# Performance work log

Measured on AMD Instinct MI355X. Metric: run time of the kernel, lower is better.

Reference implementation:

```python
import jax, jax.numpy as jnp
import numpy as np

N = 16384      # total nodes (hits)
K = 8          # n_neighbors
NB = 8         # number of graphs in batch
IN_C = 6       # in_channels
HID = 128      # hidden_channels
NCLS = 3       # num_classes
SLOPE = 0.2    # GATv2 leaky_relu negative_slope
BIG = 1e30     # mask value for cross-graph pairs


def setup_inputs() -> dict:
    key = jax.random.key(0)
    ks = jax.random.split(key, 32)
    coord = jax.random.normal(ks[0], (N, 3), dtype=jnp.float32)
    feat = jax.random.normal(ks[1], (N, IN_C), dtype=jnp.float32)
    batch = jnp.sort(jax.random.randint(ks[2], (N,), 0, NB)).astype(jnp.int32)

    def lin_w(k, fan_in, fan_out):
        return (jax.random.normal(k, (fan_in, fan_out), dtype=jnp.float32)
                * np.float32(1.0 / np.sqrt(fan_in)))

    inp = {"coord": coord, "feat": feat, "batch": batch}
    dims = [IN_C, HID, HID]  # input dim of each of the 3 GATv2 layers
    kidx = 3
    for l, din in enumerate(dims):
        inp[f"Wl{l}"] = lin_w(ks[kidx], din, HID); kidx += 1
        inp[f"bl{l}"] = jnp.zeros((HID,), jnp.float32)
        inp[f"Wr{l}"] = lin_w(ks[kidx], din, HID); kidx += 1
        inp[f"br{l}"] = jnp.zeros((HID,), jnp.float32)
        inp[f"att{l}"] = (jax.random.normal(ks[kidx], (HID,), dtype=jnp.float32)
                          * np.float32(1.0 / np.sqrt(HID))); kidx += 1
        inp[f"bias{l}"] = jnp.zeros((HID,), jnp.float32)
    inp["Wf"] = lin_w(ks[kidx], HID, NCLS)
    inp["bf"] = jnp.zeros((NCLS,), jnp.float32)
    return inp


def knn_idx(coord, batch):
    # pairwise squared distances, masked so neighbors stay within the same graph
    d2 = jnp.sum((coord[:, None, :] - coord[None, :, :]) ** 2, axis=-1)  # [N,N]
    d2 = jnp.where(batch[:, None] == batch[None, :], d2, BIG)
    _, idx = jax.lax.top_k(-d2, K)  # [N,K] nearest (includes self at dist 0)
    return idx


def gatv2_layer(x, idx, Wl, bl, Wr, br, att, bias):
    xl = x @ Wl + bl                         # [N,H] source transform
    xr = x @ Wr + br                         # [N,H] target transform
    g = xl[idx]                              # [N,K,H] gather neighbor features
    e = jax.nn.leaky_relu(g + xr[:, None, :], SLOPE)
    logits = e @ att                         # [N,K] attention scores
    alpha = jax.nn.softmax(logits, axis=1)   # softmax over each node's K nbrs
    return jnp.einsum('nk,nkh->nh', alpha, g) + bias


def reference(coord, feat, batch,
              Wl0, bl0, Wr0, br0, att0, bias0,
              Wl1, bl1, Wr1, br1, att1, bias1,
              Wl2, bl2, Wr2, br2, att2, bias2,
              Wf, bf):
    idx = knn_idx(coord, batch)
    x = jax.nn.relu(gatv2_layer(feat, idx, Wl0, bl0, Wr0, br0, att0, bias0))
    x = jax.nn.relu(gatv2_layer(x, idx, Wl1, bl1, Wr1, br1, att1, bias1))
    x = jax.nn.relu(gatv2_layer(x, idx, Wl2, bl2, Wr2, br2, att2, bias2))
    return x @ Wf + bf
```

## Files before the change

### kernel.cpp

```cpp
#include <hip/hip_runtime.h>
#include <hip/hip_bf16.h>
#include <float.h>
#include <limits.h>

#define NNODES 16384
#define KNB 8
#define HIDC 128
#define KNN_CAP 2528

__device__ __forceinline__ float wave_sum(float x) {
  x += __int_as_float(__builtin_amdgcn_update_dpp(0, __float_as_int(x), 0xB1, 0xF, 0xF, true));
  x += __int_as_float(__builtin_amdgcn_update_dpp(0, __float_as_int(x), 0x4E, 0xF, 0xF, true));
  x += __int_as_float(__builtin_amdgcn_update_dpp(0, __float_as_int(x), 0x124, 0xF, 0xF, true));
  x += __int_as_float(__builtin_amdgcn_update_dpp(0, __float_as_int(x), 0x128, 0xF, 0xF, true));
  float r0 = __int_as_float(__builtin_amdgcn_readlane(__float_as_int(x), 0));
  float r1 = __int_as_float(__builtin_amdgcn_readlane(__float_as_int(x), 16));
  float r2 = __int_as_float(__builtin_amdgcn_readlane(__float_as_int(x), 32));
  float r3 = __int_as_float(__builtin_amdgcn_readlane(__float_as_int(x), 48));
  return (r0 + r1) + (r2 + r3);
}

__device__ __forceinline__ float wave_min_f32(float x) {
  x = fminf(x, __int_as_float(__builtin_amdgcn_update_dpp(0, __float_as_int(x), 0xB1, 0xF, 0xF, true)));
  x = fminf(x, __int_as_float(__builtin_amdgcn_update_dpp(0, __float_as_int(x), 0x4E, 0xF, 0xF, true)));
  x = fminf(x, __int_as_float(__builtin_amdgcn_update_dpp(0, __float_as_int(x), 0x124, 0xF, 0xF, true)));
  x = fminf(x, __int_as_float(__builtin_amdgcn_update_dpp(0, __float_as_int(x), 0x128, 0xF, 0xF, true)));
  float r0 = __int_as_float(__builtin_amdgcn_readlane(__float_as_int(x), 0));
  float r1 = __int_as_float(__builtin_amdgcn_readlane(__float_as_int(x), 16));
  float r2 = __int_as_float(__builtin_amdgcn_readlane(__float_as_int(x), 32));
  float r3 = __int_as_float(__builtin_amdgcn_readlane(__float_as_int(x), 48));
  return fminf(fminf(r0, r1), fminf(r2, r3));
}

__device__ __forceinline__ float dist2(float ax, float ay, float az,
                                       float bx, float by, float bz) {
  float dx = ax - bx, dy = ay - by, dz = az - bz;
  return fmaf(dz, dz, fmaf(dy, dy, dx * dx));
}

#define INS8V(_d, a0, a1, a2, a3, a4, a5, a6, a7)  \
  do {                                             \
    a7 = __builtin_amdgcn_fmed3f(_d, a6, a7);      \
    a6 = __builtin_amdgcn_fmed3f(_d, a5, a6);      \
    a5 = __builtin_amdgcn_fmed3f(_d, a4, a5);      \
    a4 = __builtin_amdgcn_fmed3f(_d, a3, a4);      \
    a3 = __builtin_amdgcn_fmed3f(_d, a2, a3);      \
    a2 = __builtin_amdgcn_fmed3f(_d, a1, a2);      \
    a1 = __builtin_amdgcn_fmed3f(_d, a0, a1);      \
    a0 = fminf(a0, _d);                            \
  } while (0)

__device__ __forceinline__ float merge_T(float l0, float l1, float l2, float l3,
                                         float l4, float l5, float l6, float l7,
                                         int lane) {
  float T = 0.f;
  #pragma unroll
  for (int r = 0; r < KNB; ++r) {
    float m = wave_min_f32(l0);
    T = m;
    unsigned long long msk = __ballot(l0 == m);
    int p = (int)__builtin_ctzll(msk);
    if (lane == p) { l0 = l1; l1 = l2; l2 = l3; l3 = l4; l4 = l5; l5 = l6; l6 = l7; l7 = FLT_MAX; }
  }
  return T;
}

__device__ void knn_global_single(const float* __restrict__ coord,
                                  float qx, float qy, float qz,
                                  int s, int e, int lane,
                                  int* __restrict__ knn_row) {
  float l0 = FLT_MAX, l1 = FLT_MAX, l2 = FLT_MAX, l3 = FLT_MAX,
        l4 = FLT_MAX, l5 = FLT_MAX, l6 = FLT_MAX, l7 = FLT_MAX;
  for (int base = s; base < e; base += 64) {
    int j = base + lane;
    bool ok = j < e;
    int jc = ok ? j : s;
    float d = dist2(coord[jc*3+0], coord[jc*3+1], coord[jc*3+2], qx, qy, qz);
    d = ok ? d : FLT_MAX;
    INS8V(d, l0, l1, l2, l3, l4, l5, l6, l7);
  }
  float T = merge_T(l0, l1, l2, l3, l4, l5, l6, l7, lane);
  unsigned long long lt = (1ull << lane) - 1ull;
  int cnt = 0;
  for (int base = s; base < e; base += 64) {
    int j = base + lane;
    bool ok = j < e;
    int jc = ok ? j : s;
    float d = dist2(coord[jc*3+0], coord[jc*3+1], coord[jc*3+2], qx, qy, qz);
    bool win = ok && (d <= T);
    unsigned long long msk = __ballot(win);
    if (msk) {
      int slot = cnt + __popcll(msk & lt);
      if (win && slot < KNB) knn_row[slot] = j;
      cnt += __popcll(msk);
    }
  }
}

__global__ void seg_kernel(const int* __restrict__ batch, int* __restrict__ seg) {
  int b = threadIdx.x;
  if (b > 8) return;
  int lo = 0, hi = NNODES;
  while (lo < hi) { int m = (lo + hi) >> 1; if (batch[m] < b) lo = m + 1; else hi = m; }
  seg[b] = lo;
}

__global__ __launch_bounds__(512, 8) void knnlin_kernel(
    const float* __restrict__ coord, const int* __restrict__ batch,
    const float* __restrict__ feat,
    const float* __restrict__ Wl0, const float* __restrict__ bl0,
    const float* __restrict__ Wr0, const float* __restrict__ br0,
    const int* __restrict__ seg,
    int* __restrict__ knn, float* __restrict__ xl, float* __restrict__ xr) {
  __shared__ float4 tile[KNN_CAP];
  int t = threadIdx.x;
  int lane = t & 63;
  int wid = t >> 6;
  int n0 = blockIdx.x * 16;

  int b0 = batch[n0];
  int blast = batch[n0 + 15];
  int smin = seg[b0];
  int emax = seg[blast + 1];
  int win_end = min(emax, smin + KNN_CAP);
  int cnt_fill = win_end - smin;

  for (int i = t; i < cnt_fill; i += 512) {
    const float* cp = coord + (size_t)(smin + i) * 3;
    tile[i] = make_float4(cp[0], cp[1], cp[2], 0.f);
  }
  __syncthreads();

  int nA = n0 + wid * 2, nB = nA + 1;
  int bA = batch[nA], bB = batch[nB];
  int sA = seg[bA], eA = seg[bA + 1];
  bool fast = (bA == bB) && (eA - smin <= KNN_CAP);

  float ax = coord[nA*3+0], ay = coord[nA*3+1], az = coord[nA*3+2];
  float bx = coord[nB*3+0], by = coord[nB*3+1], bz = coord[nB*3+2];

  if (fast) {
    int lo_i = sA - smin;
    int M = eA - sA;
    int F = M >> 6, R = M & 63;

    float a0 = FLT_MAX, a1 = FLT_MAX, a2 = FLT_MAX, a3 = FLT_MAX,
          a4 = FLT_MAX, a5 = FLT_MAX, a6 = FLT_MAX, a7 = FLT_MAX;
    float b0r = FLT_MAX, b1 = FLT_MAX, b2 = FLT_MAX, b3 = FLT_MAX,
          b4 = FLT_MAX, b5 = FLT_MAX, b6 = FLT_MAX, b7 = FLT_MAX;
    if (F > 0) {
      float4 c = tile[lo_i + lane];
      for (int it = 0; it < F; ++it) {
        int nxt = (it + 1 < F) ? (it + 1) : it;
        float4 cn = tile[lo_i + nxt * 64 + lane];
        float dA = dist2(c.x, c.y, c.z, ax, ay, az);
        float dB = dist2(c.x, c.y, c.z, bx, by, bz);
        INS8V(dA, a0, a1, a2, a3, a4, a5, a6, a7);
        INS8V(dB, b0r, b1, b2, b3, b4, b5, b6, b7);
        c = cn;
      }
    }
    if (R) {
      int li = F * 64 + lane;
      bool ok = li < M;
      float4 c = tile[ok ? (lo_i + li) : lo_i];
      float dA = dist2(c.x, c.y, c.z, ax, ay, az);
      float dB = dist2(c.x, c.y, c.z, bx, by, bz);
      dA = ok ? dA : FLT_MAX;
      dB = ok ? dB : FLT_MAX;
      INS8V(dA, a0, a1, a2, a3, a4, a5, a6, a7);
      INS8V(dB, b0r, b1, b2, b3, b4, b5, b6, b7);
    }

    float TA = merge_T(a0, a1, a2, a3, a4, a5, a6, a7, lane);
    float TB = merge_T(b0r, b1, b2, b3, b4, b5, b6, b7, lane);

    unsigned long long lt = (1ull << lane) - 1ull;
    int cntA = 0, cntB = 0;
    if (F > 0) {
      float4 c = tile[lo_i + lane];
      for (int it = 0; it < F; ++it) {
        int nxt = (it + 1 < F) ? (it + 1) : it;
        float4 cn = tile[lo_i + nxt * 64 + lane];
        float dA = dist2(c.x, c.y, c.z, ax, ay, az);
        float dB = dist2(c.x, c.y, c.z, bx, by, bz);
        int gidx = sA + it * 64 + lane;
        unsigned long long mA = __ballot(dA <= TA);
        if (mA) {
          int slot = cntA + __popcll(mA & lt);
          if ((dA <= TA) && slot < KNB) knn[nA*KNB + slot] = gidx;
          cntA += __popcll(mA);
        }
        unsigned long long mB = __ballot(dB <= TB);
        if (mB) {
          int slot = cntB + __popcll(mB & lt);
          if ((dB <= TB) && slot < KNB) knn[nB*KNB + slot] = gidx;
          cntB += __popcll(mB);
        }
        if (cntA >= KNB && cntB >= KNB) break;
        c = cn;
      }
    }
    if (R && (cntA < KNB || cntB < KNB)) {
      int li = F * 64 + lane;
      bool ok = li < M;
      float4 c = tile[ok ? (lo_i + li) : lo_i];
      float dA = dist2(c.x, c.y, c.z, ax, ay, az);
      float dB = dist2(c.x, c.y, c.z, bx, by, bz);
      int gidx = sA + li;
      bool wA = ok && (dA <= TA);
      bool wB = ok && (dB <= TB);
      unsigned long long mA = __ballot(wA);
      if (mA) {
        int slot = cntA + __popcll(mA & lt);
        if (wA && slot < KNB) knn[nA*KNB + slot] = gidx;
        cntA += __popcll(mA);
      }
      unsigned long long mB = __ballot(wB);
      if (mB) {
        int slot = cntB + __popcll(mB & lt);
        if (wB && slot < KNB) knn[nB*KNB + slot] = gidx;
        cntB += __popcll(mB);
      }
    }
  } else {
    int sB2 = seg[bB], eB2 = seg[bB + 1];
    knn_global_single(coord, ax, ay, az, sA, eA, lane, knn + (size_t)nA * KNB);
    knn_global_single(coord, bx, by, bz, sB2, eB2, lane, knn + (size_t)nB * KNB);
  }

  {
    int cg = t & 63;
    bool isR = cg >= 32;
    const float* W  = isR ? Wr0 : Wl0;
    const float* bi = isR ? br0 : bl0;
    float* dst      = isR ? xr : xl;
    int wc = (cg & 31) * 4;
    float4 w0 = *(const float4*)(W + 0 * HIDC + wc);
    float4 w1 = *(const float4*)(W + 1 * HIDC + wc);
    float4 w2 = *(const float4*)(W + 2 * HIDC + wc);
    float4 w3 = *(const float4*)(W + 3 * HIDC + wc);
    float4 w4 = *(const float4*)(W + 4 * HIDC + wc);
    float4 w5 = *(const float4*)(W + 5 * HIDC + wc);
    float4 bb = *(const float4*)(bi + wc);
    #pragma unroll
    for (int s2 = 0; s2 < 2; ++s2) {
      int node = n0 + wid * 2 + s2;
      const float* fr = feat + (size_t)node * 6;
      float f0 = fr[0], f1 = fr[1], f2 = fr[2], f3 = fr[3], f4 = fr[4], f5 = fr[5];
      float4 acc = make_float4(0.f, 0.f, 0.f, 0.f);
      acc.x = fmaf(f0, w0.x, acc.x); acc.y = fmaf(f0, w0.y, acc.y);
      acc.z = fmaf(f0, w0.z, acc.z); acc.w = fmaf(f0, w0.w, acc.w);
      acc.x = fmaf(f1, w1.x, acc.x); acc.y = fmaf(f1, w1.y, acc.y);
      acc.z = fmaf(f1, w1.z, acc.z); acc.w = fmaf(f1, w1.w, acc.w);
      acc.x = fmaf(f2, w2.x, acc.x); acc.y = fmaf(f2, w2.y, acc.y);
      acc.z = fmaf(f2, w2.z, acc.z); acc.w = fmaf(f2, w2.w, acc.w);
      acc.x = fmaf(f3, w3.x, acc.x); acc.y = fmaf(f3, w3.y, acc.y);
      acc.z = fmaf(f3, w3.z, acc.z); acc.w = fmaf(f3, w3.w, acc.w);
      acc.x = fmaf(f4, w4.x, acc.x); acc.y = fmaf(f4, w4.y, acc.y);
      acc.z = fmaf(f4, w4.z, acc.z); acc.w = fmaf(f4, w4.w, acc.w);
      acc.x = fmaf(f5, w5.x, acc.x); acc.y = fmaf(f5, w5.y, acc.y);
      acc.z = fmaf(f5, w5.z, acc.z); acc.w = fmaf(f5, w5.w, acc.w);
      float4 o;
      o.x = acc.x + bb.x; o.y = acc.y + bb.y;
      o.z = acc.z + bb.z; o.w = acc.w + bb.w;
      *(float4*)(dst + (size_t)node * HIDC + wc) = o;
    }
  }
}

__global__ __launch_bounds__(256) void lin2_kernel(
    const float* __restrict__ x,
    const float* __restrict__ Wl, const float* __restrict__ bl,
    const float* __restrict__ Wr, const float* __restrict__ br,
    float* __restrict__ xl, float* __restrict__ xr) {
  __shared__ float xs[16 * HIDC];
  int t = threadIdx.x;
  int node0 = blockIdx.x * 16;
  for (int i = t; i < 16 * HIDC; i += 256) xs[i] = x[node0 * HIDC + i];
  __syncthreads();
  int cg = t & 63;
  int ng = t >> 6;
  int c0 = cg * 4;
  bool isR = (c0 >= HIDC);
  const float* W    = isR ? Wr : Wl;
  const float* bias = isR ? br : bl;
  float* dst        = isR ? xr : xl;
  int wc = isR ? (c0 - HIDC) : c0;

  float4 acc[4];
  #pragma unroll
  for (int nn = 0; nn < 4; ++nn) acc[nn] = make_float4(0.f, 0.f, 0.f, 0.f);

  for (int k0 = 0; k0 < HIDC; k0 += 4) {
    float4 xv[4];
    #pragma unroll
    for (int nn = 0; nn < 4; ++nn)
      xv[nn] = *(const float4*)&xs[(ng * 4 + nn) * HIDC + k0];
    #pragma unroll
    for (int q = 0; q < 4; ++q) {
      float4 w = *(const float4*)(W + (size_t)(k0 + q) * HIDC + wc);
      #pragma unroll
      for (int nn = 0; nn < 4; ++nn) {
        float xq = (q == 0) ? xv[nn].x : (q == 1) ? xv[nn].y : (q == 2) ? xv[nn].z : xv[nn].w;
        acc[nn].x = fmaf(xq, w.x, acc[nn].x);
        acc[nn].y = fmaf(xq, w.y, acc[nn].y);
        acc[nn].z = fmaf(xq, w.z, acc[nn].z);
        acc[nn].w = fmaf(xq, w.w, acc[nn].w);
      }
    }
  }
  float4 b4 = *(const float4*)(bias + wc);
  #pragma unroll
  for (int nn = 0; nn < 4; ++nn) {
    int node = node0 + ng * 4 + nn;
    float4 o;
    o.x = acc[nn].x + b4.x; o.y = acc[nn].y + b4.y;
    o.z = acc[nn].z + b4.z; o.w = acc[nn].w + b4.w;
    *(float4*)(dst + (size_t)node * HIDC + wc) = o;
  }
}

template<bool FINAL>
__global__ __launch_bounds__(256) void gat_attn_kernel(
    const float* __restrict__ xl, const float* __restrict__ xr,
    const int* __restrict__ knn, const float* __restrict__ att,
    const float* __restrict__ bias, float* __restrict__ xout,
    const float* __restrict__ Wf, const float* __restrict__ bf,
    float* __restrict__ out) {
  int wid = threadIdx.x >> 6;
  int lane = threadIdx.x & 63;
  int n = blockIdx.x * 4 + wid;
  int c0 = 2 * lane, c1 = 2 * lane + 1;
  float2 xr2 = *(const float2*)(xr + (size_t)n * HIDC + c0);
  float2 a2  = *(const float2*)(att + c0);
  int myj = (lane < KNB) ? knn[n * KNB + lane] : 0;
  float g0[8], g1[8], lg[8];
  #pragma unroll
  for (int k = 0; k < 8; ++k) {
    int j = __builtin_amdgcn_readlane(myj, k);
    float2 g = *(const float2*)(xl + (size_t)j * HIDC + c0);
    g0[k] = g.x; g1[k] = g.y;
    float e0 = g.x + xr2.x; e0 = (e0 > 0.f) ? e0 : 0.2f * e0;
    float e1 = g.y + xr2.y; e1 = (e1 > 0.f) ? e1 : 0.2f * e1;
    lg[k] = wave_sum(e0 * a2.x + e1 * a2.y);
  }
  float mx = lg[0];
  #pragma unroll
  for (int k = 1; k < 8; ++k) mx = fmaxf(mx, lg[k]);
  float ssum = 0.f, w[8];
  #pragma unroll
  for (int k = 0; k < 8; ++k) { w[k] = __expf(lg[k] - mx); ssum += w[k]; }
  float inv = 1.f / ssum;
  float o0 = 0.f, o1 = 0.f;
  #pragma unroll
  for (int k = 0; k < 8; ++k) { o0 += w[k] * g0[k]; o1 += w[k] * g1[k]; }
  o0 = fmaxf(fmaf(o0, inv, bias[c0]), 0.f);
  o1 = fmaxf(fmaf(o1, inv, bias[c1]), 0.f);
  if (!FINAL) {
    float2 o; o.x = o0; o.y = o1;
    *(float2*)(xout + (size_t)n * HIDC + c0) = o;
  } else {
    #pragma unroll
    for (int cls = 0; cls < 3; ++cls) {
      float p = wave_sum(o0 * Wf[c0 * 3 + cls] + o1 * Wf[c1 * 3 + cls]);
      if (lane == 0) out[n * 3 + cls] = p + bf[cls];
    }
  }
}

extern "C" void kernel_launch(void* const* d_in, const int* in_sizes, int n_in,
                              void* d_out, int out_size, void* d_ws, size_t ws_size,
                              hipStream_t stream) {
  const float* coord = (const float*)d_in[0];
  const float* feat  = (const float*)d_in[1];
  const int*   batch = (const int*)d_in[2];
  const float* Wl0 = (const float*)d_in[3];
  const float* bl0 = (const float*)d_in[4];
  const float* Wr0 = (const float*)d_in[5];
  const float* br0 = (const float*)d_in[6];
  const float* att0  = (const float*)d_in[7];
  const float* bias0 = (const float*)d_in[8];
  const float* Wl1 = (const float*)d_in[9];
  const float* bl1 = (const float*)d_in[10];
  const float* Wr1 = (const float*)d_in[11];
  const float* br1 = (const float*)d_in[12];
  const float* att1  = (const float*)d_in[13];
  const float* bias1 = (const float*)d_in[14];
  const float* Wl2 = (const float*)d_in[15];
  const float* bl2 = (const float*)d_in[16];
  const float* Wr2 = (const float*)d_in[17];
  const float* br2 = (const float*)d_in[18];
  const float* att2  = (const float*)d_in[19];
  const float* bias2 = (const float*)d_in[20];
  const float* Wf = (const float*)d_in[21];
  const float* bf = (const float*)d_in[22];
  float* out = (float*)d_out;

  char* ws = (char*)d_ws;
  int*   knn = (int*)ws;
  float* xl  = (float*)(ws + (512 << 10));
  float* xr  = xl + (size_t)NNODES * HIDC;
  float* xb0 = xr + (size_t)NNODES * HIDC;
  float* xb1 = xb0 + (size_t)NNODES * HIDC;
  int*   seg = (int*)xb1;

  seg_kernel<<<1, 16, 0, stream>>>(batch, seg);
  knnlin_kernel<<<NNODES / 16, 512, 0, stream>>>(coord, batch, feat,
                                                 Wl0, bl0, Wr0, br0, seg, knn, xl, xr);
  gat_attn_kernel<false><<<NNODES / 4, 256, 0, stream>>>(xl, xr, knn, att0, bias0, xb0,
                                                         nullptr, nullptr, nullptr);

  lin2_kernel<<<NNODES / 16, 256, 0, stream>>>(xb0, Wl1, bl1, Wr1, br1, xl, xr);
  gat_attn_kernel<false><<<NNODES / 4, 256, 0, stream>>>(xl, xr, knn, att1, bias1, xb1,
                                                         nullptr, nullptr, nullptr);

  lin2_kernel<<<NNODES / 16, 256, 0, stream>>>(xb1, Wl2, bl2, Wr2, br2, xl, xr);
  gat_attn_kernel<true><<<NNODES / 4, 256, 0, stream>>>(xl, xr, knn, att2, bias2, nullptr,
                                                        Wf, bf, out);
}
```

Measured before the change: 142.1 us.

## Map 16 lanes per node in attention and unroll kNN scan by four

```diff
diff --git a/kernel.cpp b/kernel.cpp
--- a/kernel.cpp
+++ b/kernel.cpp
@@ -7,18 +7,6 @@
 #define KNB 8
 #define HIDC 128
 #define KNN_CAP 2528
-
-__device__ __forceinline__ float wave_sum(float x) {
-  x += __int_as_float(__builtin_amdgcn_update_dpp(0, __float_as_int(x), 0xB1, 0xF, 0xF, true));
-  x += __int_as_float(__builtin_amdgcn_update_dpp(0, __float_as_int(x), 0x4E, 0xF, 0xF, true));
-  x += __int_as_float(__builtin_amdgcn_update_dpp(0, __float_as_int(x), 0x124, 0xF, 0xF, true));
-  x += __int_as_float(__builtin_amdgcn_update_dpp(0, __float_as_int(x), 0x128, 0xF, 0xF, true));
-  float r0 = __int_as_float(__builtin_amdgcn_readlane(__float_as_int(x), 0));
-  float r1 = __int_as_float(__builtin_amdgcn_readlane(__float_as_int(x), 16));
-  float r2 = __int_as_float(__builtin_amdgcn_readlane(__float_as_int(x), 32));
-  float r3 = __int_as_float(__builtin_amdgcn_readlane(__float_as_int(x), 48));
-  return (r0 + r1) + (r2 + r3);
-}
 
 __device__ __forceinline__ float wave_min_f32(float x) {
   x = fminf(x, __int_as_float(__builtin_amdgcn_update_dpp(0, __float_as_int(x), 0xB1, 0xF, 0xF, true)));
@@ -30,6 +18,14 @@
   float r2 = __int_as_float(__builtin_amdgcn_readlane(__float_as_int(x), 32));
   float r3 = __int_as_float(__builtin_amdgcn_readlane(__float_as_int(x), 48));
   return fminf(fminf(r0, r1), fminf(r2, r3));
+}
+
+__device__ __forceinline__ float sum16(float x) {
+  x += __int_as_float(__builtin_amdgcn_update_dpp(0, __float_as_int(x), 0xB1, 0xF, 0xF, true));
+  x += __int_as_float(__builtin_amdgcn_update_dpp(0, __float_as_int(x), 0x4E, 0xF, 0xF, true));
+  x += __int_as_float(__builtin_amdgcn_update_dpp(0, __float_as_int(x), 0x124, 0xF, 0xF, true));
+  x += __int_as_float(__builtin_amdgcn_update_dpp(0, __float_as_int(x), 0x128, 0xF, 0xF, true));
+  return x;
 }
 
 __device__ __forceinline__ float dist2(float ax, float ay, float az,
@@ -142,34 +138,48 @@
   if (fast) {
     int lo_i = sA - smin;
     int M = eA - sA;
-    int F = M >> 6, R = M & 63;
+    int F4 = M >> 8;
 
     float a0 = FLT_MAX, a1 = FLT_MAX, a2 = FLT_MAX, a3 = FLT_MAX,
           a4 = FLT_MAX, a5 = FLT_MAX, a6 = FLT_MAX, a7 = FLT_MAX;
     float b0r = FLT_MAX, b1 = FLT_MAX, b2 = FLT_MAX, b3 = FLT_MAX,
           b4 = FLT_MAX, b5 = FLT_MAX, b6 = FLT_MAX, b7 = FLT_MAX;
-    if (F > 0) {
-      float4 c = tile[lo_i + lane];
-      for (int it = 0; it < F; ++it) {
-        int nxt = (it + 1 < F) ? (it + 1) : it;
-        float4 cn = tile[lo_i + nxt * 64 + lane];
+    {
+      const float4* tl = tile + lo_i;
+      for (int it = 0; it < F4; ++it) {
+        float4 c0 = tl[lane];
+        float4 c1 = tl[lane + 64];
+        float4 c2 = tl[lane + 128];
+        float4 c3 = tl[lane + 192];
+        tl += 256;
+        float dA0 = dist2(c0.x, c0.y, c0.z, ax, ay, az);
+        float dB0 = dist2(c0.x, c0.y, c0.z, bx, by, bz);
+        float dA1 = dist2(c1.x, c1.y, c1.z, ax, ay, az);
+        float dB1 = dist2(c1.x, c1.y, c1.z, bx, by, bz);
+        float dA2 = dist2(c2.x, c2.y, c2.z, ax, ay, az);
+        float dB2 = dist2(c2.x, c2.y, c2.z, bx, by, bz);
+        float dA3 = dist2(c3.x, c3.y, c3.z, ax, ay, az);
+        float dB3 = dist2(c3.x, c3.y, c3.z, bx, by, bz);
+        INS8V(dA0, a0, a1, a2, a3, a4, a5, a6, a7);
+        INS8V(dB0, b0r, b1, b2, b3, b4, b5, b6, b7);
+        INS8V(dA1, a0, a1, a2, a3, a4, a5, a6, a7);
+        INS8V(dB1, b0r, b1, b2, b3, b4, b5, b6, b7);
+        INS8V(dA2, a0, a1, a2, a3, a4, a5, a6, a7);
+        INS8V(dB2, b0r, b1, b2, b3, b4, b5, b6, b7);
+        INS8V(dA3, a0, a1, a2, a3, a4, a5, a6, a7);
+        INS8V(dB3, b0r, b1, b2, b3, b4, b5, b6, b7);
+      }
+      for (int base = F4 << 8; base < M; base += 64) {
+        int lix = base + lane;
+        bool ok = lix < M;
+        float4 c = tile[ok ? (lo_i + lix) : lo_i];
         float dA = dist2(c.x, c.y, c.z, ax, ay, az);
         float dB = dist2(c.x, c.y, c.z, bx, by, bz);
+        dA = ok ? dA : FLT_MAX;
+        dB = ok ? dB : FLT_MAX;
         INS8V(dA, a0, a1, a2, a3, a4, a5, a6, a7);
         INS8V(dB, b0r, b1, b2, b3, b4, b5, b6, b7);
-        c = cn;
       }
-    }
-    if (R) {
-      int li = F * 64 + lane;
-      bool ok = li < M;
-      float4 c = tile[ok ? (lo_i + li) : lo_i];
-      float dA = dist2(c.x, c.y, c.z, ax, ay, az);
-      float dB = dist2(c.x, c.y, c.z, bx, by, bz);
-      dA = ok ? dA : FLT_MAX;
-      dB = ok ? dB : FLT_MAX;
-      INS8V(dA, a0, a1, a2, a3, a4, a5, a6, a7);
-      INS8V(dB, b0r, b1, b2, b3, b4, b5, b6, b7);
     }
 
     float TA = merge_T(a0, a1, a2, a3, a4, a5, a6, a7, lane);
@@ -177,50 +187,56 @@
 
     unsigned long long lt = (1ull << lane) - 1ull;
     int cntA = 0, cntB = 0;
-    if (F > 0) {
-      float4 c = tile[lo_i + lane];
-      for (int it = 0; it < F; ++it) {
-        int nxt = (it + 1 < F) ? (it + 1) : it;
-        float4 cn = tile[lo_i + nxt * 64 + lane];
+    {
+      const float4* t2 = tile + lo_i;
+      for (int it = 0; it < F4 && (cntA < KNB || cntB < KNB); ++it) {
+        float4 c0 = t2[lane];
+        float4 c1 = t2[lane + 64];
+        float4 c2 = t2[lane + 128];
+        float4 c3 = t2[lane + 192];
+        t2 += 256;
+        int g0 = sA + (it << 8) + lane;
+        #pragma unroll
+        for (int q = 0; q < 4; ++q) {
+          float4 c = (q == 0) ? c0 : (q == 1) ? c1 : (q == 2) ? c2 : c3;
+          int gidx = g0 + (q << 6);
+          float dA = dist2(c.x, c.y, c.z, ax, ay, az);
+          float dB = dist2(c.x, c.y, c.z, bx, by, bz);
+          unsigned long long mA = __ballot(dA <= TA);
+          if (mA) {
+            int slot = cntA + __popcll(mA & lt);
+            if ((dA <= TA) && slot < KNB) knn[nA*KNB + slot] = gidx;
+            cntA += __popcll(mA);
+          }
+          unsigned long long mB = __ballot(dB <= TB);
+          if (mB) {
+            int slot = cntB + __popcll(mB & lt);
+            if ((dB <= TB) && slot < KNB) knn[nB*KNB + slot] = gidx;
+            cntB += __popcll(mB);
+          }
+        }
+      }
+      for (int base = F4 << 8; base < M && (cntA < KNB || cntB < KNB); base += 64) {
+        int lix = base + lane;
+        bool ok = lix < M;
+        float4 c = tile[ok ? (lo_i + lix) : lo_i];
         float dA = dist2(c.x, c.y, c.z, ax, ay, az);
         float dB = dist2(c.x, c.y, c.z, bx, by, bz);
-        int gidx = sA + it * 64 + lane;
-        unsigned long long mA = __ballot(dA <= TA);
+        int gidx = sA + lix;
+        bool wA = ok && (dA <= TA);
+        bool wB = ok && (dB <= TB);
+        unsigned long long mA = __ballot(wA);
         if (mA) {
           int slot = cntA + __popcll(mA & lt);
-          if ((dA <= TA) && slot < KNB) knn[nA*KNB + slot] = gidx;
+          if (wA && slot < KNB) knn[nA*KNB + slot] = gidx;
           cntA += __popcll(mA);
         }
-        unsigned long long mB = __ballot(dB <= TB);
+        unsigned long long mB = __ballot(wB);
         if (mB) {
           int slot = cntB + __popcll(mB & lt);
-          if ((dB <= TB) && slot < KNB) knn[nB*KNB + slot] = gidx;
+          if (wB && slot < KNB) knn[nB*KNB + slot] = gidx;
           cntB += __popcll(mB);
         }
-        if (cntA >= KNB && cntB >= KNB) break;
-        c = cn;
-      }
-    }
-    if (R && (cntA < KNB || cntB < KNB)) {
-      int li = F * 64 + lane;
-      bool ok = li < M;
-      float4 c = tile[ok ? (lo_i + li) : lo_i];
-      float dA = dist2(c.x, c.y, c.z, ax, ay, az);
-      float dB = dist2(c.x, c.y, c.z, bx, by, bz);
-      int gidx = sA + li;
-      bool wA = ok && (dA <= TA);
-      bool wB = ok && (dB <= TB);
-      unsigned long long mA = __ballot(wA);
-      if (mA) {
-        int slot = cntA + __popcll(mA & lt);
-        if (wA && slot < KNB) knn[nA*KNB + slot] = gidx;
-        cntA += __popcll(mA);
-      }
-      unsigned long long mB = __ballot(wB);
-      if (mB) {
-        int slot = cntB + __popcll(mB & lt);
-        if (wB && slot < KNB) knn[nB*KNB + slot] = gidx;
-        cntB += __popcll(mB);
       }
     }
   } else {
@@ -269,7 +285,7 @@
   }
 }
 
-__global__ __launch_bounds__(256) void lin2_kernel(
+__global__ __launch_bounds__(256, 8) void lin2_kernel(
     const float* __restrict__ x,
     const float* __restrict__ Wl, const float* __restrict__ bl,
     const float* __restrict__ Wr, const float* __restrict__ br,
@@ -322,49 +338,97 @@
 }
 
 template<bool FINAL>
-__global__ __launch_bounds__(256) void gat_attn_kernel(
+__global__ __launch_bounds__(256, 8) void gat_attn_kernel(
     const float* __restrict__ xl, const float* __restrict__ xr,
     const int* __restrict__ knn, const float* __restrict__ att,
     const float* __restrict__ bias, float* __restrict__ xout,
     const float* __restrict__ Wf, const float* __restrict__ bf,
     float* __restrict__ out) {
-  int wid = threadIdx.x >> 6;
-  int lane = threadIdx.x & 63;
-  int n = blockIdx.x * 4 + wid;
-  int c0 = 2 * lane, c1 = 2 * lane + 1;
-  float2 xr2 = *(const float2*)(xr + (size_t)n * HIDC + c0);
-  float2 a2  = *(const float2*)(att + c0);
-  int myj = (lane < KNB) ? knn[n * KNB + lane] : 0;
-  float g0[8], g1[8], lg[8];
+  int t = threadIdx.x;
+  int li = t & 15;
+  int grp = t >> 4;
+  int n = blockIdx.x * 16 + grp;
+  int c0 = li * 8;
+
+  float4 xr0 = *(const float4*)(xr + (size_t)n * HIDC + c0);
+  float4 xr1 = *(const float4*)(xr + (size_t)n * HIDC + c0 + 4);
+  float4 at0 = *(const float4*)(att + c0);
+  float4 at1 = *(const float4*)(att + c0 + 4);
+  int4 j0 = *(const int4*)(knn + (size_t)n * KNB);
+  int4 j1 = *(const int4*)(knn + (size_t)n * KNB + 4);
+
+  float lg[8];
   #pragma unroll
   for (int k = 0; k < 8; ++k) {
-    int j = __builtin_amdgcn_readlane(myj, k);
-    float2 g = *(const float2*)(xl + (size_t)j * HIDC + c0);
-    g0[k] = g.x; g1[k] = g.y;
-    float e0 = g.x + xr2.x; e0 = (e0 > 0.f) ? e0 : 0.2f * e0;
-    float e1 = g.y + xr2.y; e1 = (e1 > 0.f) ? e1 : 0.2f * e1;
-    lg[k] = wave_sum(e0 * a2.x + e1 * a2.y);
-  }
+    int j = (k==0)?j0.x:(k==1)?j0.y:(k==2)?j0.z:(k==3)?j0.w
+          :(k==4)?j1.x:(k==5)?j1.y:(k==6)?j1.z:j1.w;
+    float4 g0 = *(const float4*)(xl + (size_t)j * HIDC + c0);
+    float4 g1 = *(const float4*)(xl + (size_t)j * HIDC + c0 + 4);
+    float e, p;
+    e = g0.x + xr0.x; e = e > 0.f ? e : 0.2f * e; p = e * at0.x;
+    e = g0.y + xr0.y; e = e > 0.f ? e : 0.2f * e; p = fmaf(e, at0.y, p);
+    e = g0.z + xr0.z; e = e > 0.f ? e : 0.2f * e; p = fmaf(e, at0.z, p);
+    e = g0.w + xr0.w; e = e > 0.f ? e : 0.2f * e; p = fmaf(e, at0.w, p);
+    e = g1.x + xr1.x; e = e > 0.f ? e : 0.2f * e; p = fmaf(e, at1.x, p);
+    e = g1.y + xr1.y; e = e > 0.f ? e : 0.2f * e; p = fmaf(e, at1.y, p);
+    e = g1.z + xr1.z; e = e > 0.f ? e : 0.2f * e; p = fmaf(e, at1.z, p);
+    e = g1.w + xr1.w; e = e > 0.f ? e : 0.2f * e; p = fmaf(e, at1.w, p);
+    lg[k] = sum16(p);
+  }
+
   float mx = lg[0];
   #pragma unroll
   for (int k = 1; k < 8; ++k) mx = fmaxf(mx, lg[k]);
-  float ssum = 0.f, w[8];
-  #pragma unroll
-  for (int k = 0; k < 8; ++k) { w[k] = __expf(lg[k] - mx); ssum += w[k]; }
+  float ssum = 0.f;
+  #pragma unroll
+  for (int k = 0; k < 8; ++k) { lg[k] = __expf(lg[k] - mx); ssum += lg[k]; }
   float inv = 1.f / ssum;
-  float o0 = 0.f, o1 = 0.f;
-  #pragma unroll
-  for (int k = 0; k < 8; ++k) { o0 += w[k] * g0[k]; o1 += w[k] * g1[k]; }
-  o0 = fmaxf(fmaf(o0, inv, bias[c0]), 0.f);
-  o1 = fmaxf(fmaf(o1, inv, bias[c1]), 0.f);
+
+  float4 o0 = make_float4(0.f, 0.f, 0.f, 0.f);
+  float4 o1 = make_float4(0.f, 0.f, 0.f, 0.f);
+  #pragma unroll
+  for (int k = 0; k < 8; ++k) {
+    int j = (k==0)?j0.x:(k==1)?j0.y:(k==2)?j0.z:(k==3)?j0.w
+          :(k==4)?j1.x:(k==5)?j1.y:(k==6)?j1.z:j1.w;
+    float wk = lg[k];
+    float4 g0 = *(const float4*)(xl + (size_t)j * HIDC + c0);
+    float4 g1 = *(const float4*)(xl + (size_t)j * HIDC + c0 + 4);
+    o0.x = fmaf(wk, g0.x, o0.x); o0.y = fmaf(wk, g0.y, o0.y);
+    o0.z = fmaf(wk, g0.z, o0.z); o0.w = fmaf(wk, g0.w, o0.w);
+    o1.x = fmaf(wk, g1.x, o1.x); o1.y = fmaf(wk, g1.y, o1.y);
+    o1.z = fmaf(wk, g1.z, o1.z); o1.w = fmaf(wk, g1.w, o1.w);
+  }
+  float4 b0 = *(const float4*)(bias + c0);
+  float4 b1 = *(const float4*)(bias + c0 + 4);
+  o0.x = fmaxf(fmaf(o0.x, inv, b0.x), 0.f);
+  o0.y = fmaxf(fmaf(o0.y, inv, b0.y), 0.f);
+  o0.z = fmaxf(fmaf(o0.z, inv, b0.z), 0.f);
+  o0.w = fmaxf(fmaf(o0.w, inv, b0.w), 0.f);
+  o1.x = fmaxf(fmaf(o1.x, inv, b1.x), 0.f);
+  o1.y = fmaxf(fmaf(o1.y, inv, b1.y), 0.f);
+  o1.z = fmaxf(fmaf(o1.z, inv, b1.z), 0.f);
+  o1.w = fmaxf(fmaf(o1.w, inv, b1.w), 0.f);
+
   if (!FINAL) {
-    float2 o; o.x = o0; o.y = o1;
-    *(float2*)(xout + (size_t)n * HIDC + c0) = o;
+    *(float4*)(xout + (size_t)n * HIDC + c0) = o0;
+    *(float4*)(xout + (size_t)n * HIDC + c0 + 4) = o1;
   } else {
-    #pragma unroll
-    for (int cls = 0; cls < 3; ++cls) {
-      float p = wave_sum(o0 * Wf[c0 * 3 + cls] + o1 * Wf[c1 * 3 + cls]);
-      if (lane == 0) out[n * 3 + cls] = p + bf[cls];
+    const float* wf = Wf + (size_t)c0 * 3;
+    float p0, p1, p2;
+    p0 = o0.x * wf[0];            p1 = o0.x * wf[1];            p2 = o0.x * wf[2];
+    p0 = fmaf(o0.y, wf[3], p0);   p1 = fmaf(o0.y, wf[4], p1);   p2 = fmaf(o0.y, wf[5], p2);
+    p0 = fmaf(o0.z, wf[6], p0);   p1 = fmaf(o0.z, wf[7], p1);   p2 = fmaf(o0.z, wf[8], p2);
+    p0 = fmaf(o0.w, wf[9], p0);   p1 = fmaf(o0.w, wf[10], p1);  p2 = fmaf(o0.w, wf[11], p2);
+    p0 = fmaf(o1.x, wf[12], p0);  p1 = fmaf(o1.x, wf[13], p1);  p2 = fmaf(o1.x, wf[14], p2);
+    p0 = fmaf(o1.y, wf[15], p0);  p1 = fmaf(o1.y, wf[16], p1);  p2 = fmaf(o1.y, wf[17], p2);
+    p0 = fmaf(o1.z, wf[18], p0);  p1 = fmaf(o1.z, wf[19], p1);  p2 = fmaf(o1.z, wf[20], p2);
+    p0 = fmaf(o1.w, wf[21], p0);  p1 = fmaf(o1.w, wf[22], p1);  p2 = fmaf(o1.w, wf[23], p2);
+    p0 = sum16(p0);
+    p1 = sum16(p1);
+    p2 = sum16(p2);
+    if (li < 3) {
+      float pv = (li == 0) ? p0 : (li == 1) ? p1 : p2;
+      out[(size_t)n * 3 + li] = pv + bf[li];
     }
   }
 }
@@ -408,14 +472,14 @@
   seg_kernel<<<1, 16, 0, stream>>>(batch, seg);
   knnlin_kernel<<<NNODES / 16, 512, 0, stream>>>(coord, batch, feat,
                                                  Wl0, bl0, Wr0, br0, seg, knn, xl, xr);
-  gat_attn_kernel<false><<<NNODES / 4, 256, 0, stream>>>(xl, xr, knn, att0, bias0, xb0,
-                                                         nullptr, nullptr, nullptr);
+  gat_attn_kernel<false><<<NNODES / 16, 256, 0, stream>>>(xl, xr, knn, att0, bias0, xb0,
+                                                          nullptr, nullptr, nullptr);
 
   lin2_kernel<<<NNODES / 16, 256, 0, stream>>>(xb0, Wl1, bl1, Wr1, br1, xl, xr);
-  gat_attn_kernel<false><<<NNODES / 4, 256, 0, stream>>>(xl, xr, knn, att1, bias1, xb1,
-                                                         nullptr, nullptr, nullptr);
+  gat_attn_kernel<false><<<NNODES / 16, 256, 0, stream>>>(xl, xr, knn, att1, bias1, xb1,
+                                                          nullptr, nullptr, nullptr);
 
   lin2_kernel<<<NNODES / 16, 256, 0, stream>>>(xb1, Wl2, bl2, Wr2, br2, xl, xr);
-  gat_attn_kernel<true><<<NNODES / 4, 256, 0, stream>>>(xl, xr, knn, att2, bias2, nullptr,
-                                                        Wf, bf, out);
-}
+  gat_attn_kernel<true><<<NNODES / 16, 256, 0, stream>>>(xl, xr, knn, att2, bias2, nullptr,
+                                                         Wf, bf, out);
+}
```

Result: slower. 220.3 us (+55.1%).

## Use SoA coordinate tile in LDS and unroll KNN scans by four

Applied to the files above, without the earlier changes.

```diff
diff --git a/kernel.cpp b/kernel.cpp
--- a/kernel.cpp
+++ b/kernel.cpp
@@ -112,7 +112,9 @@
     const float* __restrict__ Wr0, const float* __restrict__ br0,
     const int* __restrict__ seg,
     int* __restrict__ knn, float* __restrict__ xl, float* __restrict__ xr) {
-  __shared__ float4 tile[KNN_CAP];
+  __shared__ float xs[KNN_CAP];
+  __shared__ float ys[KNN_CAP];
+  __shared__ float zs[KNN_CAP];
   int t = threadIdx.x;
   int lane = t & 63;
   int wid = t >> 6;
@@ -127,7 +129,7 @@
 
   for (int i = t; i < cnt_fill; i += 512) {
     const float* cp = coord + (size_t)(smin + i) * 3;
-    tile[i] = make_float4(cp[0], cp[1], cp[2], 0.f);
+    xs[i] = cp[0]; ys[i] = cp[1]; zs[i] = cp[2];
   }
   __syncthreads();
 
@@ -142,34 +144,37 @@
   if (fast) {
     int lo_i = sA - smin;
     int M = eA - sA;
-    int F = M >> 6, R = M & 63;
+    int F4 = M >> 8;
 
     float a0 = FLT_MAX, a1 = FLT_MAX, a2 = FLT_MAX, a3 = FLT_MAX,
           a4 = FLT_MAX, a5 = FLT_MAX, a6 = FLT_MAX, a7 = FLT_MAX;
     float b0r = FLT_MAX, b1 = FLT_MAX, b2 = FLT_MAX, b3 = FLT_MAX,
           b4 = FLT_MAX, b5 = FLT_MAX, b6 = FLT_MAX, b7 = FLT_MAX;
-    if (F > 0) {
-      float4 c = tile[lo_i + lane];
-      for (int it = 0; it < F; ++it) {
-        int nxt = (it + 1 < F) ? (it + 1) : it;
-        float4 cn = tile[lo_i + nxt * 64 + lane];
-        float dA = dist2(c.x, c.y, c.z, ax, ay, az);
-        float dB = dist2(c.x, c.y, c.z, bx, by, bz);
+    {
+      for (int it = 0; it < F4; ++it) {
+        int base = lo_i + (it << 8) + lane;
+        #pragma unroll
+        for (int q = 0; q < 4; ++q) {
+          int i = base + (q << 6);
+          float cxv = xs[i], cyv = ys[i], czv = zs[i];
+          float dA = dist2(cxv, cyv, czv, ax, ay, az);
+          float dB = dist2(cxv, cyv, czv, bx, by, bz);
+          INS8V(dA, a0, a1, a2, a3, a4, a5, a6, a7);
+          INS8V(dB, b0r, b1, b2, b3, b4, b5, b6, b7);
+        }
+      }
+      for (int base = F4 << 8; base < M; base += 64) {
+        int lix = base + lane;
+        bool ok = lix < M;
+        int i = ok ? (lo_i + lix) : lo_i;
+        float cxv = xs[i], cyv = ys[i], czv = zs[i];
+        float dA = dist2(cxv, cyv, czv, ax, ay, az);
+        float dB = dist2(cxv, cyv, czv, bx, by, bz);
+        dA = ok ? dA : FLT_MAX;
+        dB = ok ? dB : FLT_MAX;
         INS8V(dA, a0, a1, a2, a3, a4, a5, a6, a7);
         INS8V(dB, b0r, b1, b2, b3, b4, b5, b6, b7);
-        c = cn;
       }
-    }
-    if (R) {
-      int li = F * 64 + lane;
-      bool ok = li < M;
-      float4 c = tile[ok ? (lo_i + li) : lo_i];
-      float dA = dist2(c.x, c.y, c.z, ax, ay, az);
-      float dB = dist2(c.x, c.y, c.z, bx, by, bz);
-      dA = ok ? dA : FLT_MAX;
-      dB = ok ? dB : FLT_MAX;
-      INS8V(dA, a0, a1, a2, a3, a4, a5, a6, a7);
-      INS8V(dB, b0r, b1, b2, b3, b4, b5, b6, b7);
     }
 
     float TA = merge_T(a0, a1, a2, a3, a4, a5, a6, a7, lane);
@@ -177,50 +182,53 @@
 
     unsigned long long lt = (1ull << lane) - 1ull;
     int cntA = 0, cntB = 0;
-    if (F > 0) {
-      float4 c = tile[lo_i + lane];
-      for (int it = 0; it < F; ++it) {
-        int nxt = (it + 1 < F) ? (it + 1) : it;
-        float4 cn = tile[lo_i + nxt * 64 + lane];
-        float dA = dist2(c.x, c.y, c.z, ax, ay, az);
-        float dB = dist2(c.x, c.y, c.z, bx, by, bz);
-        int gidx = sA + it * 64 + lane;
-        unsigned long long mA = __ballot(dA <= TA);
+    {
+      for (int it = 0; it < F4 && (cntA < KNB || cntB < KNB); ++it) {
+        int base = lo_i + (it << 8) + lane;
+        int g0 = sA + (it << 8) + lane;
+        #pragma unroll
+        for (int q = 0; q < 4; ++q) {
+          int i = base + (q << 6);
+          int gidx = g0 + (q << 6);
+          float cxv = xs[i], cyv = ys[i], czv = zs[i];
+          float dA = dist2(cxv, cyv, czv, ax, ay, az);
+          float dB = dist2(cxv, cyv, czv, bx, by, bz);
+          unsigned long long mA = __ballot(dA <= TA);
+          if (mA) {
+            int slot = cntA + __popcll(mA & lt);
+            if ((dA <= TA) && slot < KNB) knn[nA*KNB + slot] = gidx;
+            cntA += __popcll(mA);
+          }
+          unsigned long long mB = __ballot(dB <= TB);
+          if (mB) {
+            int slot = cntB + __popcll(mB & lt);
+            if ((dB <= TB) && slot < KNB) knn[nB*KNB + slot] = gidx;
+            cntB += __popcll(mB);
+          }
+        }
+      }
+      for (int base = F4 << 8; base < M && (cntA < KNB || cntB < KNB); base += 64) {
+        int lix = base + lane;
+        bool ok = lix < M;
+        int i = ok ? (lo_i + lix) : lo_i;
+        float cxv = xs[i], cyv = ys[i], czv = zs[i];
+        float dA = dist2(cxv, cyv, czv, ax, ay, az);
+        float dB = dist2(cxv, cyv, czv, bx, by, bz);
+        int gidx = sA + lix;
+        bool wA = ok && (dA <= TA);
+        bool wB = ok && (dB <= TB);
+        unsigned long long mA = __ballot(wA);
         if (mA) {
           int slot = cntA + __popcll(mA & lt);
-          if ((dA <= TA) && slot < KNB) knn[nA*KNB + slot] = gidx;
+          if (wA && slot < KNB) knn[nA*KNB + slot] = gidx;
           cntA += __popcll(mA);
         }
-        unsigned long long mB = __ballot(dB <= TB);
+        unsigned long long mB = __ballot(wB);
         if (mB) {
           int slot = cntB + __popcll(mB & lt);
-          if ((dB <= TB) && slot < KNB) knn[nB*KNB + slot] = gidx;
+          if (wB && slot < KNB) knn[nB*KNB + slot] = gidx;
           cntB += __popcll(mB);
         }
-        if (cntA >= KNB && cntB >= KNB) break;
-        c = cn;
-      }
-    }
-    if (R && (cntA < KNB || cntB < KNB)) {
-      int li = F * 64 + lane;
-      bool ok = li < M;
-      float4 c = tile[ok ? (lo_i + li) : lo_i];
-      float dA = dist2(c.x, c.y, c.z, ax, ay, az);
-      float dB = dist2(c.x, c.y, c.z, bx, by, bz);
-      int gidx = sA + li;
-      bool wA = ok && (dA <= TA);
-      bool wB = ok && (dB <= TB);
-      unsigned long long mA = __ballot(wA);
-      if (mA) {
-        int slot = cntA + __popcll(mA & lt);
-        if (wA && slot < KNB) knn[nA*KNB + slot] = gidx;
-        cntA += __popcll(mA);
-      }
-      unsigned long long mB = __ballot(wB);
-      if (mB) {
-        int slot = cntB + __popcll(mB & lt);
-        if (wB && slot < KNB) knn[nB*KNB + slot] = gidx;
-        cntB += __popcll(mB);
       }
     }
   } else {
@@ -274,10 +282,10 @@
     const float* __restrict__ Wl, const float* __restrict__ bl,
     const float* __restrict__ Wr, const float* __restrict__ br,
     float* __restrict__ xl, float* __restrict__ xr) {
-  __shared__ float xs[16 * HIDC];
+  __shared__ float xshm[16 * HIDC];
   int t = threadIdx.x;
   int node0 = blockIdx.x * 16;
-  for (int i = t; i < 16 * HIDC; i += 256) xs[i] = x[node0 * HIDC + i];
+  for (int i = t; i < 16 * HIDC; i += 256) xshm[i] = x[node0 * HIDC + i];
   __syncthreads();
   int cg = t & 63;
   int ng = t >> 6;
@@ -296,7 +304,7 @@
     float4 xv[4];
     #pragma unroll
     for (int nn = 0; nn < 4; ++nn)
-      xv[nn] = *(const float4*)&xs[(ng * 4 + nn) * HIDC + k0];
+      xv[nn] = *(const float4*)&xshm[(ng * 4 + nn) * HIDC + k0];
     #pragma unroll
     for (int q = 0; q < 4; ++q) {
       float4 w = *(const float4*)(W + (size_t)(k0 + q) * HIDC + wc);
```

Result: faster. 138.2 us (median of 2 runs) (-2.7%).
